# Kernel tuning notes

Measured on AMD Instinct MI355X. Metric: run time of the kernel, lower is better.

The kernel has to match this reference:

```python
import jax, jax.numpy as jnp
import numpy as np

N = 4096      # sequence length (tokens)
D = 256       # model_dim
H = 4         # num_heads
DH = D // H   # dim_per_head = 64
TOPK = 30     # dot_attention default
SCALE = float((DH // H) ** -0.5)  # torch: (key.size(-1)//num_heads)**-0.5 = 16**-0.5 = 0.25
LN_EPS = 1e-5


def setup_inputs() -> dict:
    key = jax.random.key(0)
    ks = jax.random.split(key, 11)
    s = 0.02
    return {
        "key_in":   jax.random.normal(ks[0], (N, D), jnp.float32),
        "value_in": jax.random.normal(ks[1], (N, D), jnp.float32),
        "query_in": jax.random.normal(ks[2], (N, D), jnp.float32),
        "Wq": jax.random.normal(ks[3], (D, D), jnp.float32) * s,
        "bq": jax.random.normal(ks[4], (D,), jnp.float32) * s,
        "Wk": jax.random.normal(ks[5], (D, D), jnp.float32) * s,
        "bk": jax.random.normal(ks[6], (D,), jnp.float32) * s,
        "Wv": jax.random.normal(ks[7], (D, D), jnp.float32) * s,
        "bv": jax.random.normal(ks[8], (D,), jnp.float32) * s,
        "Wo": jax.random.normal(ks[9], (D, D), jnp.float32) * s,
        "bo": jax.random.normal(ks[10], (D,), jnp.float32) * s,
        "ln_g": jnp.ones((D,), jnp.float32),
        "ln_b": jnp.zeros((D,), jnp.float32),
    }


def reference(key_in, value_in, query_in, Wq, bq, Wk, bk, Wv, bv, Wo, bo, ln_g, ln_b):
    # Projections (nn.Linear: x @ W.T + b)
    q = query_in @ Wq.T + bq            # (N, D)
    k = key_in @ Wk.T + bk
    v = value_in @ Wv.T + bv
    # view(N, H, DH).transpose(0,1) -> (H, N, DH)
    qh = q.reshape(N, H, DH).transpose(1, 0, 2)
    kh = k.reshape(N, H, DH).transpose(1, 0, 2)
    vh = v.reshape(N, H, DH).transpose(1, 0, 2)

    scores = jnp.einsum('hnd,hmd->hnm', qh, kh) * SCALE   # (H, N, N)

    # top-k mask via scatter (faithful to torch.topk + scatter_)
    idx = jax.lax.top_k(scores, TOPK)[1]                  # (H, N, TOPK)
    mask = jnp.zeros_like(scores).at[
        jnp.arange(H)[:, None, None],
        jnp.arange(N)[None, :, None],
        idx].set(1.0)
    masked = jnp.where(mask > 0, scores, -jnp.inf)
    attn = jax.nn.softmax(masked, axis=-1)                # (H, N, N); dropout p=0 -> identity

    ctx = jnp.einsum('hnm,hmd->hnd', attn, vh)            # (H, N, DH)
    ctx = ctx.transpose(1, 0, 2).reshape(N, D)

    out = ctx @ Wo.T + bo
    resid = query_in + out                                # residual is pre-projection query
    mu = resid.mean(axis=-1, keepdims=True)
    var = resid.var(axis=-1, keepdims=True)               # biased var, like torch LayerNorm
    out = (resid - mu) / jnp.sqrt(var + LN_EPS) * ln_g + ln_b
    return out, attn
```

## Files before the change

### kernel.cpp

```cpp
#include <hip/hip_runtime.h>
#include <stdint.h>

#define N_TOK 4096
#define DIM   256
#define NH    4
#define DH    64
#define TOPK  30
#define CANDN 40
#define ATT_SCALE 0.25f
#define LN_EPS 1e-5f

typedef __attribute__((ext_vector_type(8))) short bf16x8;
typedef __attribute__((ext_vector_type(4))) float f32x4;

static __device__ __forceinline__ ushort f2bf(float f) {
    uint x = __float_as_uint(f);
    return (ushort)((x + 0x7FFFu + ((x >> 16) & 1u)) >> 16);
}
static __device__ __forceinline__ bf16x8 load_frag(const ushort* p) {
    union { int4 i; bf16x8 f; } u;
    u.i = *reinterpret_cast<const int4*>(p);
    return u.f;
}
static __device__ __forceinline__ uint s16key(uint u) {
    return (u & 0x8000u) ? (u ^ 0xFFFFu) : (u | 0x8000u);
}

#define BK 32
__global__ __launch_bounds__(256) void proj_gemm_f32(
    const float* __restrict__ A, const float* __restrict__ W,
    const float* __restrict__ bias, const float* __restrict__ addX,
    float* __restrict__ outF, ushort* __restrict__ outB)
{
    __shared__ float As[BK][64 + 4];
    __shared__ float Ws[BK][64 + 4];
    const int tid = threadIdx.x;
    const int tx = tid & 15;
    const int ty = tid >> 4;
    const int i0 = blockIdx.y * 64;
    const int j0 = blockIdx.x * 64;

    float acc[4][4];
#pragma unroll
    for (int r = 0; r < 4; r++)
#pragma unroll
        for (int c = 0; c < 4; c++) acc[r][c] = 0.f;

    for (int k0 = 0; k0 < DIM; k0 += BK) {
#pragma unroll
        for (int u = 0; u < 2; u++) {
            const int f = u * 256 + tid;
            const int r = f >> 3;
            const int c = (f & 7) * 4;
            float4 va = *reinterpret_cast<const float4*>(A + (size_t)(i0 + r) * DIM + k0 + c);
            As[c + 0][r] = va.x; As[c + 1][r] = va.y;
            As[c + 2][r] = va.z; As[c + 3][r] = va.w;
            float4 vw = *reinterpret_cast<const float4*>(W + (size_t)(j0 + r) * DIM + k0 + c);
            Ws[c + 0][r] = vw.x; Ws[c + 1][r] = vw.y;
            Ws[c + 2][r] = vw.z; Ws[c + 3][r] = vw.w;
        }
        __syncthreads();
#pragma unroll
        for (int kk = 0; kk < BK; kk++) {
            const float4 a4 = *reinterpret_cast<const float4*>(&As[kk][ty * 4]);
            const float4 b4 = *reinterpret_cast<const float4*>(&Ws[kk][tx * 4]);
            const float ar[4] = {a4.x, a4.y, a4.z, a4.w};
            const float br[4] = {b4.x, b4.y, b4.z, b4.w};
#pragma unroll
            for (int r = 0; r < 4; r++)
#pragma unroll
                for (int c = 0; c < 4; c++) acc[r][c] += ar[r] * br[c];
        }
        __syncthreads();
    }

#pragma unroll
    for (int r = 0; r < 4; r++) {
        const int gi = i0 + ty * 4 + r;
#pragma unroll
        for (int c = 0; c < 4; c++) {
            const int gj = j0 + tx * 4 + c;
            float v = acc[r][c] + bias[gj];
            if (addX) v += addX[(size_t)gi * DIM + gj];
            if (outF) outF[(size_t)gi * DIM + gj] = v;
            if (outB) outB[(size_t)gi * DIM + gj] = f2bf(v);
        }
    }
}

__global__ __launch_bounds__(256) void scores_kernel(
    const ushort* __restrict__ qb, const ushort* __restrict__ kb,
    ushort* __restrict__ sb)
{
    const int lane = threadIdx.x & 63;
    const int wv   = threadIdx.x >> 6;
    const int h    = blockIdx.z;
    const int i0   = blockIdx.y * 128 + wv * 32;
    const int j0   = blockIdx.x * 128;
    const int r = lane & 15, q = lane >> 4;
    const int koff = h * DH;

    f32x4 acc[2][8];
#pragma unroll
    for (int a = 0; a < 2; a++)
#pragma unroll
        for (int b = 0; b < 8; b++) acc[a][b] = (f32x4){0.f, 0.f, 0.f, 0.f};

#pragma unroll
    for (int ks = 0; ks < 2; ks++) {
        const int kk = koff + ks * 32 + q * 8;
        bf16x8 af[2], bfr[8];
#pragma unroll
        for (int mt = 0; mt < 2; mt++)
            af[mt] = load_frag(qb + (size_t)(i0 + mt * 16 + r) * DIM + kk);
#pragma unroll
        for (int jt = 0; jt < 8; jt++)
            bfr[jt] = load_frag(kb + (size_t)(j0 + jt * 16 + r) * DIM + kk);
#pragma unroll
        for (int mt = 0; mt < 2; mt++)
#pragma unroll
            for (int jt = 0; jt < 8; jt++)
                acc[mt][jt] = __builtin_amdgcn_mfma_f32_16x16x32_bf16(
                    af[mt], bfr[jt], acc[mt][jt], 0, 0, 0);
    }

#pragma unroll
    for (int mt = 0; mt < 2; mt++)
#pragma unroll
        for (int rg = 0; rg < 4; rg++) {
            const int gi = i0 + mt * 16 + q * 4 + rg;
            ushort* row = sb + ((size_t)(h * N_TOK + gi)) * N_TOK;
#pragma unroll
            for (int jt = 0; jt < 8; jt++)
                row[j0 + jt * 16 + r] = (ushort)s16key(f2bf(acc[mt][jt][rg]));
        }
}

__global__ __launch_bounds__(256) void select_kernel(
    const ushort* __restrict__ sb, const float* __restrict__ qf,
    const float* __restrict__ kf, const float* __restrict__ vf,
    float* __restrict__ pval, int* __restrict__ pidx,
    float* __restrict__ ctx)
{
    const int lane = threadIdx.x & 63;
    const int wv   = threadIdx.x >> 6;
    const int row  = blockIdx.x * 4 + wv;
    const int h    = row >> 12;
    const int i    = row & (N_TOK - 1);
    const ushort* srow = sb + (size_t)row * N_TOK;

    __shared__ uint  hist[4][256];
    __shared__ uint  cand[4][64];
    __shared__ uint  ccnt[4];
    __shared__ float pw[4][TOPK];
    __shared__ int   jw[4][TOPK];
    __shared__ __align__(16) float qsh[4][DH];

    qsh[wv][lane] = qf[(size_t)i * DIM + h * DH + lane];
    if (lane == 0) ccnt[wv] = 0;
#pragma unroll
    for (int b = 0; b < 4; b++) hist[wv][b * 64 + lane] = 0u;

    uint kw[32];
    const int4* srow4 = reinterpret_cast<const int4*>(srow);
#pragma unroll
    for (int t = 0; t < 8; t++) {
        int4 c = srow4[t * 64 + lane];
        kw[t * 4 + 0] = (uint)c.x; kw[t * 4 + 1] = (uint)c.y;
        kw[t * 4 + 2] = (uint)c.z; kw[t * 4 + 3] = (uint)c.w;
    }

    uint mx = 0;
#pragma unroll
    for (int w = 0; w < 32; w++) {
        uint lo16 = kw[w] & 0xFFFFu, hi16 = kw[w] >> 16;
        mx = max(mx, max(lo16, hi16));
    }
#pragma unroll
    for (int off = 32; off; off >>= 1)
        mx = max(mx, (uint)__shfl_xor((int)mx, off));

    __syncthreads();

#pragma unroll
    for (int w = 0; w < 32; w++) {
        uint d0 = mx - (kw[w] & 0xFFFFu);
        uint d1 = mx - (kw[w] >> 16);
        if (d0 < 255u) atomicAdd(&hist[wv][d0], 1u);
        if (d1 < 255u) atomicAdd(&hist[wv][d1], 1u);
    }
    __syncthreads();

    const uint c0 = hist[wv][lane * 4 + 0];
    const uint c1 = hist[wv][lane * 4 + 1];
    const uint c2 = hist[wv][lane * 4 + 2];
    const uint c3 = hist[wv][lane * 4 + 3];
    const uint seg = c0 + c1 + c2 + c3;
    uint scan = seg;
#pragma unroll
    for (int d = 1; d < 64; d <<= 1) {
        uint y = (uint)__shfl_up((int)scan, d);
        if (lane >= d) scan += y;
    }
    const uint excl = scan - seg;
    const bool crossing = (excl < CANDN) && (scan >= CANDN);
    unsigned long long bal = __ballot(crossing);

    int t = 256;
    if (bal != 0ull) {
        const int srcLane = __ffsll(bal) - 1;
        int tloc = lane * 4;
        if (crossing) {
            uint cum = excl + c0;
            if (cum < CANDN) { tloc++; cum += c1;
                if (cum < CANDN) { tloc++; cum += c2;
                    if (cum < CANDN) { tloc++; } } }
        }
        t = __shfl(tloc, srcLane);
    }

    uint T;
    if (t <= 254) {
        T = mx - (uint)t;
    } else {
        uint lo = 0;
#pragma unroll
        for (int b = 15; b >= 0; b--) {
            uint trial = lo | (1u << b);
            int c = 0;
#pragma unroll
            for (int w = 0; w < 32; w++) {
                c += ((kw[w] & 0xFFFFu) >= trial) ? 1 : 0;
                c += ((kw[w] >> 16)     >= trial) ? 1 : 0;
            }
#pragma unroll
            for (int off = 32; off; off >>= 1) c += __shfl_xor(c, off);
            if (c >= CANDN) lo = trial;
        }
        T = lo;
    }

#pragma unroll
    for (int w = 0; w < 32; w++) {
        const uint lo16 = kw[w] & 0xFFFFu, hi16 = kw[w] >> 16;
        const int jbase = (w >> 2) * 512 + lane * 8 + (w & 3) * 2;
        if (lo16 >= T) {
            uint pos = atomicAdd(&ccnt[wv], 1u);
            if (pos < 64u) cand[wv][pos] = (uint)jbase;
        }
        if (hi16 >= T) {
            uint pos = atomicAdd(&ccnt[wv], 1u);
            if (pos < 64u) cand[wv][pos] = (uint)(jbase + 1);
        }
    }
    __syncthreads();
    const int m = (int)min(ccnt[wv], 64u);

    unsigned long long ukey = 0ull;
    if (lane < m) {
        const int j = (int)cand[wv][lane];
        const float4* kr = reinterpret_cast<const float4*>(kf + (size_t)j * DIM + h * DH);
        const float4* qr = reinterpret_cast<const float4*>(qsh[wv]);
        float s = 0.f;
#pragma unroll
        for (int d = 0; d < 16; d++) {
            float4 a = qr[d], bb = kr[d];
            s += a.x * bb.x; s += a.y * bb.y; s += a.z * bb.z; s += a.w * bb.w;
        }
        uint bits = __float_as_uint(s);
        uint s32 = (bits & 0x80000000u) ? ~bits : (bits | 0x80000000u);
        ukey = ((unsigned long long)s32 << 12) | (unsigned long long)(4095 - j);
    }

#pragma unroll
    for (int k = 2; k <= 64; k <<= 1) {
#pragma unroll
        for (int jj = k >> 1; jj > 0; jj >>= 1) {
            unsigned long long o = __shfl_xor(ukey, jj);
            bool keepMax = ((lane & jj) != 0) ^ ((lane & k) != 0);
            ukey = keepMax ? (ukey > o ? ukey : o) : (ukey < o ? ukey : o);
        }
    }

    const int rank = 63 - lane;
    const int jsel = 4095 - (int)(ukey & 0xFFFull);
    uint s32b = (uint)(ukey >> 12);
    uint fb = (s32b & 0x80000000u) ? (s32b ^ 0x80000000u) : ~s32b;
    const float sc = __uint_as_float(fb);
    const float stop = __shfl(sc, 63);

    float e = (rank < TOPK) ? __expf((sc - stop) * ATT_SCALE) : 0.f;
    float esum = e;
#pragma unroll
    for (int off = 32; off; off >>= 1) esum += __shfl_xor(esum, off);
    const float p = e / esum;

    if (rank < TOPK) {
        pw[wv][rank] = p; jw[wv][rank] = jsel;
        pval[(size_t)row * 32 + rank] = p;
        pidx[(size_t)row * 32 + rank] = jsel;
    }
    __syncthreads();

    float a = 0.f;
#pragma unroll
    for (int c = 0; c < TOPK; c++)
        a += pw[wv][c] * vf[(size_t)jw[wv][c] * DIM + h * DH + lane];
    ctx[(size_t)i * DIM + h * DH + lane] = a;
}

__global__ __launch_bounds__(256) void attn_write(
    const float* __restrict__ pval, const int* __restrict__ pidx,
    float* __restrict__ attnF)
{
    const int r = blockIdx.x;
    float* rowp = attnF + (size_t)r * N_TOK;
    float4* row4 = reinterpret_cast<float4*>(rowp);
    const float4 z = {0.f, 0.f, 0.f, 0.f};
#pragma unroll
    for (int t = 0; t < 4; t++) row4[t * 256 + threadIdx.x] = z;
    __syncthreads();
    if (threadIdx.x < TOPK)
        rowp[pidx[(size_t)r * 32 + threadIdx.x]] = pval[(size_t)r * 32 + threadIdx.x];
}

__global__ __launch_bounds__(64) void ln_kernel(
    float* __restrict__ resb, const float* __restrict__ g,
    const float* __restrict__ b)
{
    const int i = blockIdx.x, lane = threadIdx.x;
    float4* rowp = reinterpret_cast<float4*>(resb + (size_t)i * DIM);
    float4 x = rowp[lane];
    float s  = x.x + x.y + x.z + x.w;
    float sq = x.x * x.x + x.y * x.y + x.z * x.z + x.w * x.w;
#pragma unroll
    for (int off = 32; off; off >>= 1) {
        s  += __shfl_xor(s, off);
        sq += __shfl_xor(sq, off);
    }
    const float mu  = s * (1.f / DIM);
    const float var = sq * (1.f / DIM) - mu * mu;
    const float rstd = rsqrtf(var + LN_EPS);
    const int col = lane * 4;
    float4 o;
    o.x = (x.x - mu) * rstd * g[col + 0] + b[col + 0];
    o.y = (x.y - mu) * rstd * g[col + 1] + b[col + 1];
    o.z = (x.z - mu) * rstd * g[col + 2] + b[col + 2];
    o.w = (x.w - mu) * rstd * g[col + 3] + b[col + 3];
    rowp[lane] = o;
}

extern "C" void kernel_launch(void* const* d_in, const int* in_sizes, int n_in,
                              void* d_out, int out_size, void* d_ws, size_t ws_size,
                              hipStream_t stream)
{
    const float* key_in   = (const float*)d_in[0];
    const float* value_in = (const float*)d_in[1];
    const float* query_in = (const float*)d_in[2];
    const float* Wq = (const float*)d_in[3];
    const float* bq = (const float*)d_in[4];
    const float* Wk = (const float*)d_in[5];
    const float* bk = (const float*)d_in[6];
    const float* Wv = (const float*)d_in[7];
    const float* bv = (const float*)d_in[8];
    const float* Wo = (const float*)d_in[9];
    const float* bo = (const float*)d_in[10];
    const float* ln_g = (const float*)d_in[11];
    const float* ln_b = (const float*)d_in[12];

    float* outF  = (float*)d_out;
    float* attnF = outF + (size_t)N_TOK * DIM;

    const size_t SC = 33554432;
    ushort* sb  = (ushort*)attnF;
    float*  qf  = attnF + SC;
    float*  kf  = attnF + SC + 1048576;
    float*  vf  = attnF + SC + 2097152;
    ushort* qb  = (ushort*)(attnF + SC + 3145728);
    ushort* kb  = (ushort*)(attnF + SC + 3670016);
    float*  ctx = attnF + SC + 4194304;

    float* pval = (float*)d_ws;
    int*   pidx = (int*)d_ws + 524288;

    const dim3 gP(4, 64), bP(256);
    proj_gemm_f32<<<gP, bP, 0, stream>>>(query_in, Wq, bq, nullptr, qf, qb);
    proj_gemm_f32<<<gP, bP, 0, stream>>>(key_in,   Wk, bk, nullptr, kf, kb);
    proj_gemm_f32<<<gP, bP, 0, stream>>>(value_in, Wv, bv, nullptr, vf, nullptr);

    scores_kernel<<<dim3(32, 32, NH), 256, 0, stream>>>(qb, kb, sb);
    select_kernel<<<dim3(N_TOK * NH / 4), 256, 0, stream>>>(sb, qf, kf, vf, pval, pidx, ctx);

    proj_gemm_f32<<<gP, bP, 0, stream>>>(ctx, Wo, bo, query_in, outF, nullptr);
    ln_kernel<<<N_TOK, 64, 0, stream>>>(outF, ln_g, ln_b);

    attn_write<<<N_TOK * NH, 256, 0, stream>>>(pval, pidx, attnF);
}
```

Baseline: 475.7 us.

## Merge Q/K projections, use bf16 MFMA for V and output projections, batch attn writes

Q and K projections now run as one launch that picks its operand set by block column. The V and output projections move to a bf16 MFMA GEMM fed by a new cast kernel, and select_kernel writes the context in bf16. attn_write now builds four rows per block in shared memory and stores them with coalesced float4 writes, replacing the per-row zero fill followed by scattered global writes. The goal is fewer launches and less FP32 FMA and memory-store cost, at some risk to precision in the V and output paths.

```diff
diff --git a/kernel.cpp b/kernel.cpp
--- a/kernel.cpp
+++ b/kernel.cpp
@@ -27,18 +27,28 @@
 }
 
 #define BK 32
-__global__ __launch_bounds__(256) void proj_gemm_f32(
-    const float* __restrict__ A, const float* __restrict__ W,
-    const float* __restrict__ bias, const float* __restrict__ addX,
-    float* __restrict__ outF, ushort* __restrict__ outB)
-{
+__global__ __launch_bounds__(256) void qk_gemm_f32(
+    const float* __restrict__ query_in, const float* __restrict__ key_in,
+    const float* __restrict__ Wq, const float* __restrict__ bq,
+    const float* __restrict__ Wk, const float* __restrict__ bk,
+    float* __restrict__ qf, float* __restrict__ kf,
+    ushort* __restrict__ qb, ushort* __restrict__ kb)
+{
+    const int j0g = blockIdx.x * 64;
+    const int sel = j0g >> 8;
+    const int j0  = j0g & 255;
+    const float* A    = sel ? key_in : query_in;
+    const float* W    = sel ? Wk : Wq;
+    const float* bias = sel ? bk : bq;
+    float*  outF = sel ? kf : qf;
+    ushort* outB = sel ? kb : qb;
+
     __shared__ float As[BK][64 + 4];
     __shared__ float Ws[BK][64 + 4];
     const int tid = threadIdx.x;
     const int tx = tid & 15;
     const int ty = tid >> 4;
     const int i0 = blockIdx.y * 64;
-    const int j0 = blockIdx.x * 64;
 
     float acc[4][4];
 #pragma unroll
@@ -81,9 +91,66 @@
         for (int c = 0; c < 4; c++) {
             const int gj = j0 + tx * 4 + c;
             float v = acc[r][c] + bias[gj];
+            outF[(size_t)gi * DIM + gj] = v;
+            outB[(size_t)gi * DIM + gj] = f2bf(v);
+        }
+    }
+}
+
+__global__ __launch_bounds__(256) void cast_kernel(
+    const float* __restrict__ value_in, const float* __restrict__ Wv,
+    const float* __restrict__ Wo, ushort* __restrict__ value_b,
+    ushort* __restrict__ Wv_b, ushort* __restrict__ Wo_b)
+{
+    const int id4 = blockIdx.x * 256 + threadIdx.x;
+    const int NV = 1048576 / 4, NW = 65536 / 4;
+    const float* src; ushort* dst; int off;
+    if (id4 < NV)            { src = value_in; dst = value_b; off = id4; }
+    else if (id4 < NV + NW)  { src = Wv; dst = Wv_b; off = id4 - NV; }
+    else                     { src = Wo; dst = Wo_b; off = id4 - NV - NW; }
+    float4 v = reinterpret_cast<const float4*>(src)[off];
+    ushort4 o = {f2bf(v.x), f2bf(v.y), f2bf(v.z), f2bf(v.w)};
+    reinterpret_cast<ushort4*>(dst)[off] = o;
+}
+
+__global__ __launch_bounds__(256) void mfma_gemm(
+    const ushort* __restrict__ A, const ushort* __restrict__ B,
+    const float* __restrict__ bias, const float* __restrict__ addX,
+    float* __restrict__ outF)
+{
+    const int lane = threadIdx.x & 63;
+    const int wv   = threadIdx.x >> 6;
+    const int i0   = blockIdx.y * 64 + wv * 16;
+    const int j0   = blockIdx.x * 64;
+    const int r = lane & 15, q = lane >> 4;
+
+    f32x4 acc[4];
+#pragma unroll
+    for (int b = 0; b < 4; b++) acc[b] = (f32x4){0.f, 0.f, 0.f, 0.f};
+
+#pragma unroll
+    for (int ks = 0; ks < 8; ks++) {
+        const int kk = ks * 32 + q * 8;
+        bf16x8 af = load_frag(A + (size_t)(i0 + r) * DIM + kk);
+        bf16x8 bfr[4];
+#pragma unroll
+        for (int jt = 0; jt < 4; jt++)
+            bfr[jt] = load_frag(B + (size_t)(j0 + jt * 16 + r) * DIM + kk);
+#pragma unroll
+        for (int jt = 0; jt < 4; jt++)
+            acc[jt] = __builtin_amdgcn_mfma_f32_16x16x32_bf16(af, bfr[jt], acc[jt], 0, 0, 0);
+    }
+
+#pragma unroll
+    for (int jt = 0; jt < 4; jt++) {
+        const int gj = j0 + jt * 16 + r;
+        const float bv = bias[gj];
+#pragma unroll
+        for (int rg = 0; rg < 4; rg++) {
+            const int gi = i0 + q * 4 + rg;
+            float v = acc[jt][rg] + bv;
             if (addX) v += addX[(size_t)gi * DIM + gj];
-            if (outF) outF[(size_t)gi * DIM + gj] = v;
-            if (outB) outB[(size_t)gi * DIM + gj] = f2bf(v);
+            outF[(size_t)gi * DIM + gj] = v;
         }
     }
 }
@@ -140,7 +207,7 @@
     const ushort* __restrict__ sb, const float* __restrict__ qf,
     const float* __restrict__ kf, const float* __restrict__ vf,
     float* __restrict__ pval, int* __restrict__ pidx,
-    float* __restrict__ ctx)
+    ushort* __restrict__ ctxb)
 {
     const int lane = threadIdx.x & 63;
     const int wv   = threadIdx.x >> 6;
@@ -306,22 +373,34 @@
 #pragma unroll
     for (int c = 0; c < TOPK; c++)
         a += pw[wv][c] * vf[(size_t)jw[wv][c] * DIM + h * DH + lane];
-    ctx[(size_t)i * DIM + h * DH + lane] = a;
+    ctxb[(size_t)i * DIM + h * DH + lane] = f2bf(a);
 }
 
 __global__ __launch_bounds__(256) void attn_write(
     const float* __restrict__ pval, const int* __restrict__ pidx,
     float* __restrict__ attnF)
 {
-    const int r = blockIdx.x;
-    float* rowp = attnF + (size_t)r * N_TOK;
-    float4* row4 = reinterpret_cast<float4*>(rowp);
+    __shared__ __align__(16) float rb[4][N_TOK];
+    const int tid = threadIdx.x;
+    const int r0 = blockIdx.x * 4;
+
+    float4* rb4 = reinterpret_cast<float4*>(&rb[0][0]);
     const float4 z = {0.f, 0.f, 0.f, 0.f};
 #pragma unroll
-    for (int t = 0; t < 4; t++) row4[t * 256 + threadIdx.x] = z;
-    __syncthreads();
-    if (threadIdx.x < TOPK)
-        rowp[pidx[(size_t)r * 32 + threadIdx.x]] = pval[(size_t)r * 32 + threadIdx.x];
+    for (int t = 0; t < 16; t++) rb4[t * 256 + tid] = z;
+    __syncthreads();
+    if (tid < 4 * TOPK) {
+        const int w = tid / TOPK, c = tid % TOPK;
+        rb[w][pidx[(size_t)(r0 + w) * 32 + c]] = pval[(size_t)(r0 + w) * 32 + c];
+    }
+    __syncthreads();
+#pragma unroll
+    for (int w = 0; w < 4; w++) {
+        float4* grow = reinterpret_cast<float4*>(attnF + (size_t)(r0 + w) * N_TOK);
+#pragma unroll
+        for (int t = 0; t < 4; t++)
+            grow[t * 256 + tid] = rb4[w * 1024 + t * 256 + tid];
+    }
 }
 
 __global__ __launch_bounds__(64) void ln_kernel(
@@ -372,27 +451,32 @@
     float* attnF = outF + (size_t)N_TOK * DIM;
 
     const size_t SC = 33554432;
-    ushort* sb  = (ushort*)attnF;
-    float*  qf  = attnF + SC;
-    float*  kf  = attnF + SC + 1048576;
-    float*  vf  = attnF + SC + 2097152;
-    ushort* qb  = (ushort*)(attnF + SC + 3145728);
-    ushort* kb  = (ushort*)(attnF + SC + 3670016);
-    float*  ctx = attnF + SC + 4194304;
-
-    float* pval = (float*)d_ws;
-    int*   pidx = (int*)d_ws + 524288;
-
-    const dim3 gP(4, 64), bP(256);
-    proj_gemm_f32<<<gP, bP, 0, stream>>>(query_in, Wq, bq, nullptr, qf, qb);
-    proj_gemm_f32<<<gP, bP, 0, stream>>>(key_in,   Wk, bk, nullptr, kf, kb);
-    proj_gemm_f32<<<gP, bP, 0, stream>>>(value_in, Wv, bv, nullptr, vf, nullptr);
+    ushort* sb   = (ushort*)attnF;
+    float*  qf   = attnF + SC;
+    float*  kf   = attnF + SC + 1048576;
+    float*  vf   = attnF + SC + 2097152;
+    ushort* qb   = (ushort*)(attnF + SC + 3145728);
+    ushort* kb   = (ushort*)(attnF + SC + 3670016);
+    ushort* ctxb = (ushort*)(attnF + SC + 4194304);
+
+    float*  pval    = (float*)d_ws;
+    int*    pidx    = (int*)d_ws + 524288;
+    ushort* value_b = (ushort*)((char*)d_ws + (4u << 20));
+    ushort* Wv_b    = (ushort*)((char*)d_ws + (6u << 20));
+    ushort* Wo_b    = (ushort*)((char*)d_ws + (6u << 20) + 131072);
+
+    cast_kernel<<<dim3((1048576 + 65536 + 65536) / 4 / 256), 256, 0, stream>>>(
+        value_in, Wv, Wo, value_b, Wv_b, Wo_b);
+    qk_gemm_f32<<<dim3(8, 64), 256, 0, stream>>>(
+        query_in, key_in, Wq, bq, Wk, bk, qf, kf, qb, kb);
+    mfma_gemm<<<dim3(4, 64), 256, 0, stream>>>(value_b, Wv_b, bv, nullptr, vf);
 
     scores_kernel<<<dim3(32, 32, NH), 256, 0, stream>>>(qb, kb, sb);
-    select_kernel<<<dim3(N_TOK * NH / 4), 256, 0, stream>>>(sb, qf, kf, vf, pval, pidx, ctx);
-
-    proj_gemm_f32<<<gP, bP, 0, stream>>>(ctx, Wo, bo, query_in, outF, nullptr);
+    select_kernel<<<dim3(N_TOK * NH / 4), 256, 0, stream>>>(
+        sb, qf, kf, vf, pval, pidx, ctxb);
+
+    mfma_gemm<<<dim3(4, 64), 256, 0, stream>>>(ctxb, Wo_b, bo, query_in, outF);
     ln_kernel<<<N_TOK, 64, 0, stream>>>(outF, ln_g, ln_b);
 
-    attn_write<<<N_TOK * NH, 256, 0, stream>>>(pval, pidx, attnF);
-}
+    attn_write<<<N_TOK * NH / 4, 256, 0, stream>>>(pval, pidx, attnF);
+}
```

Result: faster. 440.5 us (-7.4%).
